# Kernel tuning notes

Measured on AMD Instinct MI355X. Metric: run time of the kernel, lower is better.

The kernel has to match this reference:

```python
import jax, jax.numpy as jnp
import numpy as np


def setup_inputs() -> dict:
    key = jax.random.key(0)
    k0, k1, k2, k3 = jax.random.split(key, 4)
    B, N, QS, KS = 32, 10, 128, 256
    C, H, Wd = 512, 32, 32
    qu = jax.random.normal(k0, (B, N, QS), dtype=jnp.float32)
    k = jax.random.normal(k1, (B, N, KS), dtype=jnp.float32)
    v = jax.random.normal(k2, (B, N, C, H, Wd), dtype=jnp.float32)
    W = jax.random.normal(k3, (KS, QS), dtype=jnp.float32) / np.sqrt(QS)
    b = jnp.zeros((KS,), dtype=jnp.float32)
    return {"qu": qu, "k": k, "v": v, "W": W, "b": b}


def reference(qu, k, v, W, b):
    # query projection: [B, N, key_size]
    query = jnp.einsum('bnq,kq->bnk', qu, W) + b
    # attn_orig = bmm(k, query^T): [B, N_k, N_q]
    attn = jnp.einsum('bkd,bqd->bkq', k, query)
    N = attn.shape[1]
    i = jnp.arange(N - 1)[:, None]   # rows of diagonal-removed matrix
    j = jnp.arange(N)[None, :]       # query columns
    # diagonal removal: del[i,j] = attn[i,j] if j>i else attn[i+1,j]  -> [B, N-1, N]
    r_del = i + (j <= i).astype(jnp.int32)
    dd = attn[:, r_del, jnp.broadcast_to(j, r_del.shape)]
    # softmax over the N-1 keys (torch dim=1)
    S = jax.nn.softmax(dd, axis=1)
    # re-insert zero diagonal: app[i,j] = S[i,j] if j>i; S[i-1,j] if j<i; 0 if j==i
    i2 = jnp.arange(N)[:, None]
    r_app = jnp.clip(i2 - (j < i2).astype(jnp.int32), 0, N - 2)
    app = jnp.where(j != i2, S[:, r_app, jnp.broadcast_to(j, r_app.shape)], 0.0)
    # weighted sum of per-agent feature maps (replaces 6D broadcast-expand-sum)
    out = jnp.einsum('bkq,bkchw->bqchw', app, v)
    return out, app
```

## Files before the change

kernel.cpp:

```cpp
#include <hip/hip_runtime.h>
#include <math.h>

#define B_  32
#define NN  10
#define QS  128
#define KS  256
#define CHW  524288
#define CHW4 131072

typedef float f4 __attribute__((ext_vector_type(4)));

__global__ __launch_bounds__(256) void attn_weights_kernel(
    const float* __restrict__ qu, const float* __restrict__ kin,
    const float* __restrict__ W, const float* __restrict__ bias,
    float* __restrict__ app_out)
{
    const int b = blockIdx.x;
    const int t = threadIdx.x;

    __shared__ __align__(16) float s_qu[NN * QS];
    __shared__ __align__(16) float s_k[NN * KS];
    __shared__ __align__(16) float s_query[NN * KS];
    __shared__ float s_attn[NN * NN];

    for (int i = t; i < NN * QS; i += 256) s_qu[i] = qu[(size_t)b * NN * QS + i];
    for (int i = t; i < NN * KS; i += 256) s_k[i]  = kin[(size_t)b * NN * KS + i];
    __syncthreads();

    {
        float acc[NN];
        const float bv = bias[t];
        #pragma unroll
        for (int n = 0; n < NN; ++n) acc[n] = bv;
        const float4* wrow = (const float4*)(W + (size_t)t * QS);
        const float4* qu4  = (const float4*)s_qu;
        for (int q4 = 0; q4 < QS / 4; ++q4) {
            const float4 w = wrow[q4];
            #pragma unroll
            for (int n = 0; n < NN; ++n) {
                const float4 u = qu4[n * (QS / 4) + q4];
                acc[n] += w.x * u.x + w.y * u.y + w.z * u.z + w.w * u.w;
            }
        }
        #pragma unroll
        for (int n = 0; n < NN; ++n) s_query[n * KS + t] = acc[n];
    }
    __syncthreads();

    if (t < NN * NN) {
        const int i = t / NN, j = t % NN;
        float s = 0.f;
        for (int d = 0; d < KS; ++d) s += s_k[i * KS + d] * s_query[j * KS + d];
        s_attn[i * NN + j] = s;
    }
    __syncthreads();

    if (t < NN) {
        const int j = t;
        float m = -1e30f;
        #pragma unroll
        for (int i = 0; i < NN; ++i)
            if (i != j) m = fmaxf(m, s_attn[i * NN + j]);
        float denom = 0.f;
        #pragma unroll
        for (int i = 0; i < NN; ++i)
            if (i != j) denom += expf(s_attn[i * NN + j] - m);
        const float inv = 1.f / denom;
        #pragma unroll
        for (int i = 0; i < NN; ++i) {
            const float a = (i == j) ? 0.f : expf(s_attn[i * NN + j] - m) * inv;
            app_out[(size_t)b * NN * NN + i * NN + j] = a;
        }
    }
}

__global__ __launch_bounds__(256) void wsum_kernel(
    const f4* __restrict__ v, const float* __restrict__ app,
    f4* __restrict__ out)
{
    const int b = blockIdx.y;
    __shared__ float s_app[NN * NN];
    if (threadIdx.x < NN * NN) s_app[threadIdx.x] = app[(size_t)b * NN * NN + threadIdx.x];
    __syncthreads();

    const int pos = blockIdx.x * 256 + threadIdx.x;
    const f4* vb = v   + (size_t)b * NN * CHW4 + pos;
    f4*       ob = out + (size_t)b * NN * CHW4 + pos;

    f4 vv[NN];
    #pragma unroll
    for (int kk = 0; kk < NN; ++kk)
        vv[kk] = __builtin_nontemporal_load(&vb[(size_t)kk * CHW4]);

    #pragma unroll
    for (int q = 0; q < NN; ++q) {
        f4 acc = (f4)(0.f);
        #pragma unroll
        for (int kk = 0; kk < NN; ++kk) {
            const float a = s_app[kk * NN + q];
            acc.x += a * vv[kk].x;
            acc.y += a * vv[kk].y;
            acc.z += a * vv[kk].z;
            acc.w += a * vv[kk].w;
        }
        __builtin_nontemporal_store(acc, &ob[(size_t)q * CHW4]);
    }
}

extern "C" void kernel_launch(void* const* d_in, const int* in_sizes, int n_in,
                              void* d_out, int out_size, void* d_ws, size_t ws_size,
                              hipStream_t stream) {
    const float* qu   = (const float*)d_in[0];
    const float* k    = (const float*)d_in[1];
    const float* v    = (const float*)d_in[2];
    const float* W    = (const float*)d_in[3];
    const float* bias = (const float*)d_in[4];

    float* out = (float*)d_out;
    float* app = out + (size_t)B_ * NN * CHW;

    attn_weights_kernel<<<B_, 256, 0, stream>>>(qu, k, W, bias, app);
    wsum_kernel<<<dim3(CHW4 / 256, B_), 256, 0, stream>>>(
        (const f4*)v, app, (f4*)out);
}
```

Before: 251.0 us.

## Make wsum kernel persistent with double-buffered register prefetch across chunks

The weighted-sum kernel now launches 64 blocks per batch instead of 512. Each thread processes 8 strided chunks and prefetches the next chunk's 10 agent vectors into registers while computing and storing the current one. The aim is to cut block launch overhead and keep more loads in flight per thread. In exchange, register pressure roughly doubles, which may reduce occupancy, and the grid becomes smaller.

Measured after the change: 268.8 us. 7.1% more time.

```diff
diff --git a/kernel.cpp b/kernel.cpp
--- a/kernel.cpp
+++ b/kernel.cpp
@@ -7,6 +7,9 @@
 #define KS  256
 #define CHW  524288
 #define CHW4 131072
+#define BLKS_PER_B 64
+#define CHUNK 16384
+#define NCHUNK 8
 
 typedef float f4 __attribute__((ext_vector_type(4)));
 
@@ -74,24 +77,14 @@
     }
 }
 
-__global__ __launch_bounds__(256) void wsum_kernel(
-    const f4* __restrict__ v, const float* __restrict__ app,
-    f4* __restrict__ out)
-{
-    const int b = blockIdx.y;
-    __shared__ float s_app[NN * NN];
-    if (threadIdx.x < NN * NN) s_app[threadIdx.x] = app[(size_t)b * NN * NN + threadIdx.x];
-    __syncthreads();
-
-    const int pos = blockIdx.x * 256 + threadIdx.x;
-    const f4* vb = v   + (size_t)b * NN * CHW4 + pos;
-    f4*       ob = out + (size_t)b * NN * CHW4 + pos;
-
-    f4 vv[NN];
+__device__ __forceinline__ void load_chunk(f4* vv, const f4* __restrict__ vb, int pos) {
     #pragma unroll
     for (int kk = 0; kk < NN; ++kk)
-        vv[kk] = __builtin_nontemporal_load(&vb[(size_t)kk * CHW4]);
+        vv[kk] = __builtin_nontemporal_load(&vb[(size_t)kk * CHW4 + pos]);
+}
 
+__device__ __forceinline__ void compute_store(const f4* vv, const float* s_app,
+                                              f4* __restrict__ ob, int pos) {
     #pragma unroll
     for (int q = 0; q < NN; ++q) {
         f4 acc = (f4)(0.f);
@@ -103,7 +96,35 @@
             acc.z += a * vv[kk].z;
             acc.w += a * vv[kk].w;
         }
-        __builtin_nontemporal_store(acc, &ob[(size_t)q * CHW4]);
+        __builtin_nontemporal_store(acc, &ob[(size_t)q * CHW4 + pos]);
+    }
+}
+
+__global__ __launch_bounds__(256) void wsum_kernel(
+    const f4* __restrict__ v, const float* __restrict__ app,
+    f4* __restrict__ out)
+{
+    const int b      = blockIdx.x >> 6;
+    const int blkInB = blockIdx.x & 63;
+
+    __shared__ float s_app[NN * NN];
+    if (threadIdx.x < NN * NN) s_app[threadIdx.x] = app[(size_t)b * NN * NN + threadIdx.x];
+    __syncthreads();
+
+    const size_t base = (size_t)b * NN * CHW4;
+    const f4* vb = v   + base;
+    f4*       ob = out + base;
+    const int pos0 = blkInB * 256 + threadIdx.x;
+
+    f4 vvA[NN], vvB[NN];
+    load_chunk(vvA, vb, pos0);
+
+    #pragma unroll
+    for (int c = 0; c < NCHUNK; c += 2) {
+        load_chunk(vvB, vb, pos0 + (c + 1) * CHUNK);
+        compute_store(vvA, s_app, ob, pos0 + c * CHUNK);
+        if (c + 2 < NCHUNK) load_chunk(vvA, vb, pos0 + (c + 2) * CHUNK);
+        compute_store(vvB, s_app, ob, pos0 + (c + 1) * CHUNK);
     }
 }
 
@@ -120,6 +141,5 @@
     float* app = out + (size_t)B_ * NN * CHW;
 
     attn_weights_kernel<<<B_, 256, 0, stream>>>(qu, k, W, bias, app);
-    wsum_kernel<<<dim3(CHW4 / 256, B_), 256, 0, stream>>>(
-        (const f4*)v, app, (f4*)out);
+    wsum_kernel<<<B_ * BLKS_PER_B, 256, 0, stream>>>((const f4*)v, app, (f4*)out);
 }
```
